# Kernel tuning notes

Hardware: AMD Instinct MI355X
Metric: run time of the kernel (lower is better)

## Reference

```python
import jax, jax.numpy as jnp
import numpy as np

B, DIM_IN, DIM_OUT, K, EMBED, N, S = 32, 32, 32, 2, 16, 2048, 12


def setup_inputs() -> dict:
    key = jax.random.key(0)
    ks = jax.random.split(key, 12)
    sc = 0.1
    return {
        "x": jax.random.normal(ks[0], (B, DIM_IN, N, S), dtype=jnp.float32),
        "node_embeddings": jax.random.normal(ks[1], (N, EMBED), dtype=jnp.float32),
        "node_embeddings2": jax.random.normal(ks[2], (N, EMBED), dtype=jnp.float32),
        "weights_pool": jax.random.normal(ks[3], (EMBED, K + 1, DIM_IN, DIM_OUT), dtype=jnp.float32) * sc,
        "weights_pool2": jax.random.normal(ks[4], (EMBED, K + 1, DIM_IN, DIM_OUT), dtype=jnp.float32) * sc,
        "bias_pool": jax.random.normal(ks[5], (EMBED, DIM_OUT), dtype=jnp.float32) * sc,
        "bias_pool2": jax.random.normal(ks[6], (EMBED, DIM_OUT), dtype=jnp.float32) * sc,
        "fc0_w": jax.random.normal(ks[7], (1, S), dtype=jnp.float32) * sc,
        "fc0_b": jnp.zeros((1,), dtype=jnp.float32),
        "fc1_w": jax.random.normal(ks[8], (EMBED, N), dtype=jnp.float32) * sc,
        "fc1_b": jnp.zeros((EMBED,), dtype=jnp.float32),
        "fc2_w": jax.random.normal(ks[9], (EMBED, DIM_IN), dtype=jnp.float32) * sc,
        "fc2_b": jnp.zeros((EMBED,), dtype=jnp.float32),
    }


def _mlp(x, fc0_w, fc0_b, fc1_w, fc1_b, fc2_w, fc2_b):
    # x: [B, i, n, s] -> use first batch element, as in the torch code
    h = x[0]                                        # [i, n, s]
    h = jnp.tanh((h @ fc0_w.T + fc0_b).squeeze(-1))  # [i, n]
    h = jnp.tanh(h @ fc1_w.T + fc1_b)                # [i, d]
    h = h.T                                          # [d, i]
    h = jnp.tanh(h @ fc2_w.T + fc2_b)                # [d, d]
    return h


def reference(x, node_embeddings, node_embeddings2, weights_pool, weights_pool2,
              bias_pool, bias_pool2, fc0_w, fc0_b, fc1_w, fc1_b, fc2_w, fc2_b):
    m = _mlp(x, fc0_w, fc0_b, fc1_w, fc1_b, fc2_w, fc2_b)          # [d, d]
    logits = jax.nn.relu((node_embeddings @ m) @ node_embeddings2.T)  # [n, n]
    support = jax.nn.softmax(logits, axis=1)                        # [n, n]

    # k-hop powers of the dynamic adjacency (k is a small static int)
    support_set = [jnp.eye(N, dtype=support.dtype)]
    for _ in range(K):
        support_set.append(support_set[-1] @ support)
    supports = jnp.stack(support_set, axis=0)                       # [K+1, n, n]

    # node-embedding-generated weights and bias
    weights = (jnp.einsum('nd,dkio->nkio', node_embeddings, weights_pool)
               + jnp.einsum('nd,dkio->nkio', node_embeddings2, weights_pool2))  # [n,K+1,i,o]
    bias = node_embeddings @ bias_pool + node_embeddings2 @ bias_pool2          # [n, o]

    x_g = jnp.einsum('knm,bims->bknis', supports, x)                # [b,K+1,n,i,s]
    x_gconv = jnp.einsum('bknis,nkio->bsno', x_g, weights) + bias   # [b,s,n,o]
    out = jnp.transpose(x_gconv, (0, 3, 2, 1))                      # [b,o,n,s]
    # dropout is identity in eval mode
    return out
```

## Files before the change

kernel.cpp:

```cpp
#include <hip/hip_runtime.h>


typedef float  f32x4  __attribute__((ext_vector_type(4)));
typedef __bf16 bf16x8 __attribute__((ext_vector_type(8)));
typedef unsigned short u16;

#define GLOAD16(gp, lp) __builtin_amdgcn_global_load_lds( \
    (const __attribute__((address_space(1))) void*)(gp),  \
    (__attribute__((address_space(3))) void*)(lp), 16, 0, 0)

__device__ __forceinline__ u16 f2bf(float f){
  union { float f; unsigned u; } v; v.f = f;
  unsigned u = v.u;
  u += 0x7fffu + ((u >> 16) & 1u);
  return (u16)(u >> 16);
}
__device__ __forceinline__ float bf2f(u16 h){
  union { unsigned u; float f; } v; v.u = ((unsigned)h) << 16;
  return v.f;
}
__device__ __forceinline__ float2 unp2(unsigned u){
  union { unsigned q; float f; } a, b;
  a.q = u << 16; b.q = u & 0xffff0000u;
  return make_float2(a.f, b.f);
}

__global__ void k_h1(const float* __restrict__ x, const float* __restrict__ fc0w,
                     const float* __restrict__ fc0b, float* __restrict__ h1){
  int g = blockIdx.x * 256 + threadIdx.x;
  const float* xp = x + (long)g * 12;
  float s = fc0b[0];
  #pragma unroll
  for (int j = 0; j < 12; j++) s += xp[j] * fc0w[j];
  h1[g] = tanhf(s);
}

__global__ __launch_bounds__(256) void k_h2a(const float* __restrict__ h1,
                                             const float* __restrict__ fc1w,
                                             float* __restrict__ h2raw){
  __shared__ float red[4];
  int id = blockIdx.x;
  int i = id >> 4, d = id & 15;
  int t = threadIdx.x;
  const float* hp = h1 + i * 2048;
  const float* wp = fc1w + d * 2048;
  float s = 0.f;
  for (int nn = t; nn < 2048; nn += 256) s += hp[nn] * wp[nn];
  for (int off = 32; off > 0; off >>= 1) s += __shfl_down(s, off, 64);
  if ((t & 63) == 0) red[t >> 6] = s;
  __syncthreads();
  if (t == 0) h2raw[id] = red[0] + red[1] + red[2] + red[3];
}

__global__ void k_h2b(const float* __restrict__ h2raw, const float* __restrict__ fc1b,
                      const float* __restrict__ fc2w, const float* __restrict__ fc2b,
                      float* __restrict__ mmat){
  __shared__ float h2[512];
  int t = threadIdx.x;
  {
    int d = t & 15;
    h2[t] = tanhf(h2raw[t] + fc1b[d]);
  }
  __syncthreads();
  if (t < 256){
    int dd = t >> 4, e = t & 15;
    float s2 = fc2b[e];
    #pragma unroll
    for (int ii = 0; ii < 32; ii++) s2 += h2[ii * 16 + dd] * fc2w[e * 32 + ii];
    mmat[dd * 16 + e] = tanhf(s2);
  }
}

__global__ __launch_bounds__(256) void k_support(const float* __restrict__ E1,
                                                 const float* __restrict__ E2,
                                                 const float* __restrict__ mmat,
                                                 u16* __restrict__ sup){
  __shared__ float ml[256];
  __shared__ float tv[16];
  __shared__ float red[8];
  int n = blockIdx.x, t = threadIdx.x;
  ml[t] = mmat[t];
  __syncthreads();
  if (t < 16){
    float s = 0.f;
    const float* er = E1 + n * 16;
    #pragma unroll
    for (int d = 0; d < 16; d++) s += er[d] * ml[d * 16 + t];
    tv[t] = s;
  }
  __syncthreads();
  float lmax = -1e30f;
  float lv[8];
  #pragma unroll
  for (int p = 0; p < 8; p++){
    int j = t + p * 256;
    const float* e2 = E2 + j * 16;
    float s = 0.f;
    #pragma unroll
    for (int d = 0; d < 16; d++) s += tv[d] * e2[d];
    s = fmaxf(s, 0.f);
    lv[p] = s;
    lmax = fmaxf(lmax, s);
  }
  for (int off = 32; off > 0; off >>= 1) lmax = fmaxf(lmax, __shfl_down(lmax, off, 64));
  if ((t & 63) == 0) red[t >> 6] = lmax;
  __syncthreads();
  if (t == 0) red[0] = fmaxf(fmaxf(red[0], red[1]), fmaxf(red[2], red[3]));
  __syncthreads();
  float mx = red[0];
  float lsum = 0.f;
  #pragma unroll
  for (int p = 0; p < 8; p++){ float e = __expf(lv[p] - mx); lv[p] = e; lsum += e; }
  for (int off = 32; off > 0; off >>= 1) lsum += __shfl_down(lsum, off, 64);
  if ((t & 63) == 0) red[4 + (t >> 6)] = lsum;
  __syncthreads();
  if (t == 0) red[4] = red[4] + red[5] + red[6] + red[7];
  __syncthreads();
  float inv = 1.f / red[4];
  #pragma unroll
  for (int p = 0; p < 8; p++) sup[(long)n * 2048 + t + p * 256] = f2bf(lv[p] * inv);
}

__global__ __launch_bounds__(256) void k_xbt2(const float* __restrict__ x,
                                              u16* __restrict__ Xb,
                                              u16* __restrict__ Xbt){
  __shared__ u16 tile[64][65];
  int cT = blockIdx.x * 64;
  int mT = blockIdx.y * 64;
  int t = threadIdx.x;
  int r = t >> 6, cc = t & 63;
  int cg = cT + cc;
  int bi = cg / 12, s = cg - bi * 12;
  long xoff = (long)bi * 24576 + s;
  #pragma unroll
  for (int p = 0; p < 16; p++){
    int rr = p * 4 + r;
    u16 v = f2bf(x[xoff + (long)(mT + rr) * 12]);
    tile[rr][cc] = v;
    Xb[(long)(mT + rr) * 12288 + cg] = v;
  }
  __syncthreads();
  #pragma unroll
  for (int p = 0; p < 16; p++){
    int rr = p * 4 + r;
    Xbt[(long)(cT + rr) * 2048 + mT + cc] = tile[cc][rr];
  }
}

__global__ __launch_bounds__(256) void k_wb2(const float* __restrict__ E1, const float* __restrict__ E2,
                                             const float* __restrict__ P1, const float* __restrict__ P2,
                                             const float* __restrict__ BP1, const float* __restrict__ BP2,
                                             float* __restrict__ W, float* __restrict__ biasN){
  int bid = blockIdx.x, t = threadIdx.x;
  if (bid < 6144){
    int nb = bid & 511, rb = bid >> 9;
    int n = nb * 4 + (t >> 6);
    int r4 = rb * 64 + (t & 63);
    const float* e1 = E1 + n * 16;
    const float* e2 = E2 + n * 16;
    f32x4 s = {0.f, 0.f, 0.f, 0.f};
    #pragma unroll
    for (int d = 0; d < 16; d++){
      f32x4 p1 = *(const f32x4*)(P1 + d * 3072 + r4 * 4);
      f32x4 p2 = *(const f32x4*)(P2 + d * 3072 + r4 * 4);
      s += p1 * e1[d] + p2 * e2[d];
    }
    *(f32x4*)(W + (long)n * 3072 + r4 * 4) = s;
  } else {
    int e = (bid - 6144) * 256 + t;
    int n = e >> 5, o = e & 31;
    const float* e1 = E1 + n * 16;
    const float* e2 = E2 + n * 16;
    float s = 0.f;
    #pragma unroll
    for (int d = 0; d < 16; d++) s += e1[d] * BP1[d * 32 + o] + e2[d] * BP2[d * 32 + o];
    biasN[e] = s;
  }
}

__global__ __launch_bounds__(512, 2) void k_gemm(const u16* __restrict__ A,
                                                 const u16* __restrict__ Bt,
                                                 u16* __restrict__ Cd,
                                                 u16* __restrict__ Ct,
                                                 int writeT){
  __shared__ u16 lds[65536];
  int tid  = threadIdx.x;
  int wave = tid >> 6, lane = tid & 63;
  int l15 = lane & 15, q = lane >> 4, l7 = l15 & 7;
  int wm = wave >> 2, wn = wave & 3;

  int lin  = blockIdx.y * 48 + blockIdx.x;
  int xcd  = lin & 7;
  int slot = lin >> 3;
  int yN   = slot / 6;
  int xN   = (slot - yN * 6) * 8 + xcd;
  long mBase = (long)yN * 256;
  long cBase = (long)xN * 256;

  f32x4 acc[8][4];
  #pragma unroll
  for (int t2 = 0; t2 < 8; t2++)
    #pragma unroll
    for (int u2 = 0; u2 < 4; u2++) acc[t2][u2] = (f32x4){0.f, 0.f, 0.f, 0.f};

  int Lrow = tid >> 3;
  int cel  = (tid & 7) ^ (Lrow & 7);
  const u16* gAp = A  + (mBase + Lrow) * 2048 + cel * 8;
  const u16* gBp = Bt + (cBase + Lrow) * 2048 + cel * 8;

#define GL_A(nx, ko, r) GLOAD16(gAp + (r) * (64 * 2048) + (ko), \
                                lds + (nx) + (r) * 4096 + wave * 512)
#define GL_B(nx, ko, r) GLOAD16(gBp + (r) * (64 * 2048) + (ko), \
                                lds + (nx) + 16384 + (r) * 4096 + wave * 512)

#define LDA(dst, mq) do { \
    _Pragma("unroll") \
    for (int t2 = 0; t2 < 4; t2++){ \
      int row = wm * 128 + ((mq) * 4 + t2) * 16 + l15; \
      _Pragma("unroll") \
      for (int kk = 0; kk < 2; kk++) \
        dst[t2][kk] = *(const bf16x8*)&lds[bA + row * 64 + (((kk << 2) | q) ^ l7) * 8]; \
    } } while(0)

#define LDB(nq) do { \
    _Pragma("unroll") \
    for (int u2 = 0; u2 < 2; u2++){ \
      int row = wn * 64 + ((nq) * 2 + u2) * 16 + l15; \
      _Pragma("unroll") \
      for (int kk = 0; kk < 2; kk++) \
        bb[u2][kk] = *(const bf16x8*)&lds[bB + row * 64 + (((kk << 2) | q) ^ l7) * 8]; \
    } } while(0)

#define MFMA_Q(AF, mq, nq) do { \
    __builtin_amdgcn_s_setprio(1); \
    _Pragma("unroll") \
    for (int t2 = 0; t2 < 4; t2++) \
      _Pragma("unroll") \
      for (int u2 = 0; u2 < 2; u2++) \
        _Pragma("unroll") \
        for (int kk = 0; kk < 2; kk++) \
          acc[(mq) * 4 + t2][(nq) * 2 + u2] = __builtin_amdgcn_mfma_f32_16x16x32_bf16( \
              AF[t2][kk], bb[u2][kk], acc[(mq) * 4 + t2][(nq) * 2 + u2], 0, 0, 0); \
    __builtin_amdgcn_s_setprio(0); \
  } while(0)

  GL_B(0, 0, 0); GL_B(0, 0, 1); GL_B(0, 0, 2); GL_B(0, 0, 3);
  GL_A(0, 0, 0); GL_A(0, 0, 2); GL_A(0, 0, 1); GL_A(0, 0, 3);

  for (int t = 0; t < 32; t++){
    const int bA = (t & 1) ? 32768 : 0;
    const int bB = bA + 16384;
    const int nx = (t & 1) ? 0 : 32768;
    const long ko = (long)(t + 1) * 64;
    bf16x8 aA[4][2], aB[4][2], bb[2][2];
    asm volatile("s_waitcnt vmcnt(0)" ::: "memory");
    __builtin_amdgcn_s_barrier();
    LDA(aA, 0);
    LDB(0);
    if (t < 31){ GL_B(nx, ko, 0); GL_B(nx, ko, 1); GL_B(nx, ko, 2); GL_B(nx, ko, 3); }
    __builtin_amdgcn_s_barrier();
    MFMA_Q(aA, 0, 0);
    __builtin_amdgcn_s_barrier();
    LDA(aB, 1);
    if (t < 31){ GL_A(nx, ko, 0); GL_A(nx, ko, 2); }
    __builtin_amdgcn_s_barrier();
    MFMA_Q(aB, 1, 0);
    __builtin_amdgcn_s_barrier();
    LDB(1);
    if (t < 31){ GL_A(nx, ko, 1); GL_A(nx, ko, 3); }
    __builtin_amdgcn_s_barrier();
    MFMA_Q(aB, 1, 1);
    __builtin_amdgcn_s_barrier();
    MFMA_Q(aA, 0, 1);
    __builtin_amdgcn_s_barrier();
  }
  asm volatile("s_waitcnt vmcnt(0)" ::: "memory");
  __syncthreads();

  #pragma unroll
  for (int t2 = 0; t2 < 8; t2++){
    int m0 = wm * 128 + t2 * 16 + q * 4;
    #pragma unroll
    for (int u2 = 0; u2 < 4; u2++){
      int c = wn * 64 + u2 * 16 + l15;
      ushort4 v = make_ushort4(f2bf(acc[t2][u2][0]), f2bf(acc[t2][u2][1]),
                               f2bf(acc[t2][u2][2]), f2bf(acc[t2][u2][3]));
      int sw = ((m0 >> 3) ^ (c & 7) ^ ((c >> 3) & 7));
      *(ushort4*)&lds[c * 256 + (sw << 3) + (m0 & 7)] = v;
    }
  }
  __syncthreads();
  int rr = tid >> 5;
  int ch = tid & 31;
  if (writeT){
    #pragma unroll
    for (int p = 0; p < 16; p++){
      int r = p * 16 + rr;
      uint4 v = *(const uint4*)&lds[r * 256 + ((ch ^ (r & 7) ^ ((r >> 3) & 7)) << 3)];
      *(uint4*)&Ct[(cBase + r) * 2048 + mBase + ch * 8] = v;
    }
  }
  #pragma unroll
  for (int p = 0; p < 16; p++){
    int m = p * 16 + rr;
    int msw = (m >> 3), ml = m & 7;
    unsigned w[4];
    #pragma unroll
    for (int jj = 0; jj < 4; jj++){
      int c0 = ch * 8 + jj * 2, c1 = c0 + 1;
      unsigned lo = lds[c0 * 256 + (((msw ^ (c0 & 7) ^ (ch & 7)) << 3)) + ml];
      unsigned hi = lds[c1 * 256 + (((msw ^ (c1 & 7) ^ (ch & 7)) << 3)) + ml];
      w[jj] = lo | (hi << 16);
    }
    uint4 v = make_uint4(w[0], w[1], w[2], w[3]);
    *(uint4*)&Cd[(mBase + m) * 12288 + cBase + ch * 8] = v;
  }
#undef GL_A
#undef GL_B
#undef LDA
#undef LDB
#undef MFMA_Q
}

__global__ __launch_bounds__(256, 4) void k_final(const u16* __restrict__ G0,
                                                  const u16* __restrict__ G1,
                                                  const u16* __restrict__ G2,
                                                  const float* __restrict__ W,
                                                  const float* __restrict__ biasN,
                                                  float* __restrict__ out){
  __shared__ __align__(16) u16 gs[32 * 400];
  __shared__ __align__(16) float ws4[1024];
  __shared__ float bbuf[32];
  int bid = blockIdx.x;
  int n = (bid & 7) * 256 + (bid >> 3);
  int t = threadIdx.x;
  int b = t >> 3, oc = t & 7;
  f32x4 acc[4][3];
  #pragma unroll
  for (int jo = 0; jo < 4; jo++)
    #pragma unroll
    for (int v = 0; v < 3; v++) acc[jo][v] = (f32x4){0.f, 0.f, 0.f, 0.f};

  const u16* srcs[3] = {G0, G1, G2};
  for (int k = 0; k < 3; k++){
    __syncthreads();
    const uint4* src = (const uint4*)(srcs[k] + (long)n * 12288);
    #pragma unroll
    for (int p = 0; p < 6; p++){
      int c = t + p * 256;
      int br = c / 48, wi = c - br * 48;
      *(uint4*)&gs[br * 400 + wi * 8] = src[c];
    }
    const float4* wsrc = (const float4*)(W + (long)n * 3072 + k * 1024);
    *(float4*)&ws4[t * 4] = wsrc[t];
    if (k == 0 && t < 8) *(float4*)&bbuf[t * 4] = ((const float4*)(biasN + (long)n * 32))[t];
    __syncthreads();

    const u16* gp = gs + b * 400;
    #pragma unroll 4
    for (int ii = 0; ii < 16; ii++){
      uint4 A  = *(const uint4*)&gp[ii * 24];
      uint4 Bc = *(const uint4*)&gp[ii * 24 + 8];
      uint4 Cc = *(const uint4*)&gp[ii * 24 + 16];
      float2 p0 = unp2(A.x),  p1 = unp2(A.y),  p2 = unp2(A.z),  p3 = unp2(A.w);
      float2 p4 = unp2(Bc.x), p5 = unp2(Bc.y), p6 = unp2(Bc.z), p7 = unp2(Bc.w);
      float2 p8 = unp2(Cc.x), p9 = unp2(Cc.y), pa = unp2(Cc.z), pb = unp2(Cc.w);
      f32x4 G0v0 = (f32x4){p0.x, p0.y, p1.x, p1.y};
      f32x4 G0v1 = (f32x4){p2.x, p2.y, p3.x, p3.y};
      f32x4 G0v2 = (f32x4){p4.x, p4.y, p5.x, p5.y};
      f32x4 G1v0 = (f32x4){p6.x, p6.y, p7.x, p7.y};
      f32x4 G1v1 = (f32x4){p8.x, p8.y, p9.x, p9.y};
      f32x4 G1v2 = (f32x4){pa.x, pa.y, pb.x, pb.y};
      #pragma unroll
      for (int jo = 0; jo < 4; jo++){
        float w0 = ws4[(ii * 2)     * 32 + oc + jo * 8];
        float w1 = ws4[(ii * 2 + 1) * 32 + oc + jo * 8];
        acc[jo][0] += G0v0 * w0;
        acc[jo][1] += G0v1 * w0;
        acc[jo][2] += G0v2 * w0;
        acc[jo][0] += G1v0 * w1;
        acc[jo][1] += G1v1 * w1;
        acc[jo][2] += G1v2 * w1;
      }
    }
  }
  #pragma unroll
  for (int jo = 0; jo < 4; jo++){
    int o = oc + jo * 8;
    float bv = bbuf[o];
    f32x4 bs = {bv, bv, bv, bv};
    long base = ((long)(b * 32 + o) * 2048 + n) * 12;
    *(f32x4*)(out + base)     = acc[jo][0] + bs;
    *(f32x4*)(out + base + 4) = acc[jo][1] + bs;
    *(f32x4*)(out + base + 8) = acc[jo][2] + bs;
  }
}

extern "C" void kernel_launch(void* const* d_in, const int* in_sizes, int n_in,
                              void* d_out, int out_size, void* d_ws, size_t ws_size,
                              hipStream_t stream){
  const float* x    = (const float*)d_in[0];
  const float* E1   = (const float*)d_in[1];
  const float* E2   = (const float*)d_in[2];
  const float* P1   = (const float*)d_in[3];
  const float* P2   = (const float*)d_in[4];
  const float* BP1  = (const float*)d_in[5];
  const float* BP2  = (const float*)d_in[6];
  const float* fc0w = (const float*)d_in[7];
  const float* fc0b = (const float*)d_in[8];
  const float* fc1w = (const float*)d_in[9];
  const float* fc1b = (const float*)d_in[10];
  const float* fc2w = (const float*)d_in[11];
  const float* fc2b = (const float*)d_in[12];
  float* out = (float*)d_out;

  char* ws = (char*)d_ws;
  size_t off = 0;
  auto carve = [&](size_t bytes) -> char* {
    char* p = ws + off;
    off += (bytes + 255) & ~(size_t)255;
    return p;
  };
  float* h1            = (float*)carve((size_t)65536 * 4);
  float* h2raw         = (float*)carve((size_t)512 * 4);
  float* mmat          = (float*)carve((size_t)256 * 4);
  u16* sup             = (u16*)carve((size_t)2048 * 2048 * 2);
  u16* Xbt             = (u16*)carve((size_t)12288 * 2048 * 2);
  u16* Xb              = (u16*)carve((size_t)2048 * 12288 * 2);
  u16* G1t             = (u16*)carve((size_t)12288 * 2048 * 2);
  u16* G1              = (u16*)carve((size_t)2048 * 12288 * 2);
  float* W             = (float*)carve((size_t)2048 * 3072 * 4);
  float* biasN         = (float*)carve((size_t)2048 * 32 * 4);
  u16* G2              = Xbt;
  (void)ws_size; (void)in_sizes; (void)n_in; (void)out_size;

  k_h1     <<<256, 256, 0, stream>>>(x, fc0w, fc0b, h1);
  k_h2a    <<<512, 256, 0, stream>>>(h1, fc1w, h2raw);
  k_h2b    <<<1, 512, 0, stream>>>(h2raw, fc1b, fc2w, fc2b, mmat);
  k_support<<<2048, 256, 0, stream>>>(E1, E2, mmat, sup);
  k_xbt2   <<<dim3(192, 32), 256, 0, stream>>>(x, Xb, Xbt);
  k_wb2    <<<6400, 256, 0, stream>>>(E1, E2, P1, P2, BP1, BP2, W, biasN);
  k_gemm   <<<dim3(48, 8), 512, 0, stream>>>(sup, Xbt, G1, G1t, 1);
  k_gemm   <<<dim3(48, 8), 512, 0, stream>>>(sup, G1t, G2, G1t, 0);
  k_final  <<<2048, 256, 0, stream>>>(Xb, G1, G2, W, biasN, out);
}
```

Measured before the change: 615.8 us.

## Enlarge GEMM tile to 256x384 for a single-wave grid with finer load waits

The bf16 support GEMM tile grows from 256x256 to 256x384, so each launch uses 256 blocks instead of 384. On a 256-CU part this removes the 1.5-wave tail, and each loaded A tile is reused over more columns. The main loop now uses partial vmcnt waits so the second-half A rows can still be arriving while the first half is consumed. The epilogue writes output in two 192-column halves to fit the LDS staging buffer. In exchange, LDS use rises to 160 KB, which allows only one block per CU. Register pressure also grows with 192 accumulator VGPRs, and the last iteration issues redundant wrapped loads.

```diff
diff --git a/kernel.cpp b/kernel.cpp
--- a/kernel.cpp
+++ b/kernel.cpp
@@ -183,25 +183,25 @@
                                                  u16* __restrict__ Cd,
                                                  u16* __restrict__ Ct,
                                                  int writeT){
-  __shared__ u16 lds[65536];
+  __shared__ u16 lds[81920];
   int tid  = threadIdx.x;
   int wave = tid >> 6, lane = tid & 63;
   int l15 = lane & 15, q = lane >> 4, l7 = l15 & 7;
   int wm = wave >> 2, wn = wave & 3;
 
-  int lin  = blockIdx.y * 48 + blockIdx.x;
+  int lin  = blockIdx.y * 32 + blockIdx.x;
   int xcd  = lin & 7;
   int slot = lin >> 3;
-  int yN   = slot / 6;
-  int xN   = (slot - yN * 6) * 8 + xcd;
+  int yN   = slot >> 2;
+  int xN   = (slot & 3) * 8 + xcd;
   long mBase = (long)yN * 256;
-  long cBase = (long)xN * 256;
-
-  f32x4 acc[8][4];
+  long cBase = (long)xN * 384;
+
+  f32x4 acc[8][6];
   #pragma unroll
   for (int t2 = 0; t2 < 8; t2++)
     #pragma unroll
-    for (int u2 = 0; u2 < 4; u2++) acc[t2][u2] = (f32x4){0.f, 0.f, 0.f, 0.f};
+    for (int u2 = 0; u2 < 6; u2++) acc[t2][u2] = (f32x4){0.f, 0.f, 0.f, 0.f};
 
   int Lrow = tid >> 3;
   int cel  = (tid & 7) ^ (Lrow & 7);
@@ -222,16 +222,16 @@
         dst[t2][kk] = *(const bf16x8*)&lds[bA + row * 64 + (((kk << 2) | q) ^ l7) * 8]; \
     } } while(0)
 
-#define LDB(nq) do { \
+#define LDB(dst, nq2) do { \
     _Pragma("unroll") \
     for (int u2 = 0; u2 < 2; u2++){ \
-      int row = wn * 64 + ((nq) * 2 + u2) * 16 + l15; \
+      int row = wn * 96 + ((nq2) * 2 + u2) * 16 + l15; \
       _Pragma("unroll") \
       for (int kk = 0; kk < 2; kk++) \
-        bb[u2][kk] = *(const bf16x8*)&lds[bB + row * 64 + (((kk << 2) | q) ^ l7) * 8]; \
+        dst[u2][kk] = *(const bf16x8*)&lds[bB + row * 64 + (((kk << 2) | q) ^ l7) * 8]; \
     } } while(0)
 
-#define MFMA_Q(AF, mq, nq) do { \
+#define MFMA_Q(AF, mq, BB, nb) do { \
     __builtin_amdgcn_s_setprio(1); \
     _Pragma("unroll") \
     for (int t2 = 0; t2 < 4; t2++) \
@@ -239,81 +239,100 @@
       for (int u2 = 0; u2 < 2; u2++) \
         _Pragma("unroll") \
         for (int kk = 0; kk < 2; kk++) \
-          acc[(mq) * 4 + t2][(nq) * 2 + u2] = __builtin_amdgcn_mfma_f32_16x16x32_bf16( \
-              AF[t2][kk], bb[u2][kk], acc[(mq) * 4 + t2][(nq) * 2 + u2], 0, 0, 0); \
+          acc[(mq) * 4 + t2][(nb) + u2] = __builtin_amdgcn_mfma_f32_16x16x32_bf16( \
+              AF[t2][kk], BB[u2][kk], acc[(mq) * 4 + t2][(nb) + u2], 0, 0, 0); \
     __builtin_amdgcn_s_setprio(0); \
   } while(0)
 
-  GL_B(0, 0, 0); GL_B(0, 0, 1); GL_B(0, 0, 2); GL_B(0, 0, 3);
+  GL_B(0, 0, 0); GL_B(0, 0, 1); GL_B(0, 0, 2);
+  GL_B(0, 0, 3); GL_B(0, 0, 4); GL_B(0, 0, 5);
   GL_A(0, 0, 0); GL_A(0, 0, 2); GL_A(0, 0, 1); GL_A(0, 0, 3);
 
   for (int t = 0; t < 32; t++){
-    const int bA = (t & 1) ? 32768 : 0;
+    const int bA = (t & 1) ? 40960 : 0;
     const int bB = bA + 16384;
-    const int nx = (t & 1) ? 0 : 32768;
-    const long ko = (long)(t + 1) * 64;
-    bf16x8 aA[4][2], aB[4][2], bb[2][2];
-    asm volatile("s_waitcnt vmcnt(0)" ::: "memory");
-    __builtin_amdgcn_s_barrier();
-    LDA(aA, 0);
-    LDB(0);
-    if (t < 31){ GL_B(nx, ko, 0); GL_B(nx, ko, 1); GL_B(nx, ko, 2); GL_B(nx, ko, 3); }
-    __builtin_amdgcn_s_barrier();
-    MFMA_Q(aA, 0, 0);
-    __builtin_amdgcn_s_barrier();
-    LDA(aB, 1);
-    if (t < 31){ GL_A(nx, ko, 0); GL_A(nx, ko, 2); }
-    __builtin_amdgcn_s_barrier();
-    MFMA_Q(aB, 1, 0);
-    __builtin_amdgcn_s_barrier();
-    LDB(1);
-    if (t < 31){ GL_A(nx, ko, 1); GL_A(nx, ko, 3); }
-    __builtin_amdgcn_s_barrier();
-    MFMA_Q(aB, 1, 1);
-    __builtin_amdgcn_s_barrier();
-    MFMA_Q(aA, 0, 1);
-    __builtin_amdgcn_s_barrier();
+    const int nx = (t & 1) ? 0 : 40960;
+    const long ko = (long)((t + 1) & 31) * 64;
+    bf16x8 aA0[4][2], aA1[4][2], bb0[2][2], bb1[2][2], bb2[2][2];
+    asm volatile("s_waitcnt vmcnt(2)" ::: "memory");
+    __builtin_amdgcn_s_barrier();
+    LDA(aA0, 0);
+    LDB(bb0, 0);
+    GL_B(nx, ko, 0); GL_B(nx, ko, 1);
+    __builtin_amdgcn_s_barrier();
+    MFMA_Q(aA0, 0, bb0, 0);
+    __builtin_amdgcn_s_barrier();
+    LDB(bb1, 1);
+    GL_B(nx, ko, 2); GL_B(nx, ko, 3);
+    __builtin_amdgcn_s_barrier();
+    MFMA_Q(aA0, 0, bb1, 2);
+    __builtin_amdgcn_s_barrier();
+    LDB(bb2, 2);
+    GL_B(nx, ko, 4); GL_B(nx, ko, 5);
+    __builtin_amdgcn_s_barrier();
+    MFMA_Q(aA0, 0, bb2, 4);
+    asm volatile("s_waitcnt vmcnt(6)" ::: "memory");
+    __builtin_amdgcn_s_barrier();
+    LDA(aA1, 1);
+    GL_A(nx, ko, 0); GL_A(nx, ko, 2);
+    __builtin_amdgcn_s_barrier();
+    MFMA_Q(aA1, 1, bb2, 4);
+    __builtin_amdgcn_s_barrier();
+    GL_A(nx, ko, 1); GL_A(nx, ko, 3);
+    __builtin_amdgcn_s_barrier();
+    MFMA_Q(aA1, 1, bb1, 2);
+    __builtin_amdgcn_s_barrier();
+    MFMA_Q(aA1, 1, bb0, 0);
   }
   asm volatile("s_waitcnt vmcnt(0)" ::: "memory");
-  __syncthreads();
-
-  #pragma unroll
-  for (int t2 = 0; t2 < 8; t2++){
-    int m0 = wm * 128 + t2 * 16 + q * 4;
-    #pragma unroll
-    for (int u2 = 0; u2 < 4; u2++){
-      int c = wn * 64 + u2 * 16 + l15;
-      ushort4 v = make_ushort4(f2bf(acc[t2][u2][0]), f2bf(acc[t2][u2][1]),
-                               f2bf(acc[t2][u2][2]), f2bf(acc[t2][u2][3]));
-      int sw = ((m0 >> 3) ^ (c & 7) ^ ((c >> 3) & 7));
-      *(ushort4*)&lds[c * 256 + (sw << 3) + (m0 & 7)] = v;
-    }
-  }
-  __syncthreads();
-  int rr = tid >> 5;
-  int ch = tid & 31;
-  if (writeT){
-    #pragma unroll
-    for (int p = 0; p < 16; p++){
-      int r = p * 16 + rr;
-      uint4 v = *(const uint4*)&lds[r * 256 + ((ch ^ (r & 7) ^ ((r >> 3) & 7)) << 3)];
-      *(uint4*)&Ct[(cBase + r) * 2048 + mBase + ch * 8] = v;
-    }
-  }
-  #pragma unroll
-  for (int p = 0; p < 16; p++){
-    int m = p * 16 + rr;
-    int msw = (m >> 3), ml = m & 7;
-    unsigned w[4];
-    #pragma unroll
-    for (int jj = 0; jj < 4; jj++){
-      int c0 = ch * 8 + jj * 2, c1 = c0 + 1;
-      unsigned lo = lds[c0 * 256 + (((msw ^ (c0 & 7) ^ (ch & 7)) << 3)) + ml];
-      unsigned hi = lds[c1 * 256 + (((msw ^ (c1 & 7) ^ (ch & 7)) << 3)) + ml];
-      w[jj] = lo | (hi << 16);
-    }
-    uint4 v = make_uint4(w[0], w[1], w[2], w[3]);
-    *(uint4*)&Cd[(mBase + m) * 12288 + cBase + ch * 8] = v;
+  __builtin_amdgcn_sched_barrier(0);
+  __syncthreads();
+
+  for (int hc = 0; hc < 2; hc++){
+    if (hc) __syncthreads();
+    if ((wn >> 1) == hc){
+      int wnl = wn & 1;
+      #pragma unroll
+      for (int t2 = 0; t2 < 8; t2++){
+        int m0 = wm * 128 + t2 * 16 + q * 4;
+        #pragma unroll
+        for (int u2 = 0; u2 < 6; u2++){
+          int lc = wnl * 96 + u2 * 16 + l15;
+          ushort4 v = make_ushort4(f2bf(acc[t2][u2][0]), f2bf(acc[t2][u2][1]),
+                                   f2bf(acc[t2][u2][2]), f2bf(acc[t2][u2][3]));
+          int sw = ((m0 >> 3) ^ (lc & 7) ^ ((lc >> 3) & 7));
+          *(ushort4*)&lds[lc * 256 + (sw << 3) + (m0 & 7)] = v;
+        }
+      }
+    }
+    __syncthreads();
+    int rr = tid >> 5;
+    int ch = tid & 31;
+    if (writeT){
+      #pragma unroll
+      for (int p = 0; p < 12; p++){
+        int r = p * 16 + rr;
+        uint4 v = *(const uint4*)&lds[r * 256 + ((ch ^ (r & 7) ^ ((r >> 3) & 7)) << 3)];
+        *(uint4*)&Ct[(cBase + hc * 192 + r) * 2048 + mBase + ch * 8] = v;
+      }
+    }
+    if (ch < 24){
+      #pragma unroll
+      for (int p = 0; p < 16; p++){
+        int m = p * 16 + rr;
+        int msw = (m >> 3), ml = m & 7;
+        unsigned w[4];
+        #pragma unroll
+        for (int jj = 0; jj < 4; jj++){
+          int c0 = ch * 8 + jj * 2, c1 = c0 + 1;
+          unsigned lo = lds[c0 * 256 + (((msw ^ (c0 & 7) ^ (ch & 7)) << 3)) + ml];
+          unsigned hi = lds[c1 * 256 + (((msw ^ (c1 & 7) ^ (ch & 7)) << 3)) + ml];
+          w[jj] = lo | (hi << 16);
+        }
+        uint4 v = make_uint4(w[0], w[1], w[2], w[3]);
+        *(uint4*)&Cd[(mBase + m) * 12288 + cBase + hc * 192 + ch * 8] = v;
+      }
+    }
   }
 #undef GL_A
 #undef GL_B
@@ -440,7 +459,7 @@
   k_support<<<2048, 256, 0, stream>>>(E1, E2, mmat, sup);
   k_xbt2   <<<dim3(192, 32), 256, 0, stream>>>(x, Xb, Xbt);
   k_wb2    <<<6400, 256, 0, stream>>>(E1, E2, P1, P2, BP1, BP2, W, biasN);
-  k_gemm   <<<dim3(48, 8), 512, 0, stream>>>(sup, Xbt, G1, G1t, 1);
-  k_gemm   <<<dim3(48, 8), 512, 0, stream>>>(sup, G1t, G2, G1t, 0);
+  k_gemm   <<<dim3(32, 8), 512, 0, stream>>>(sup, Xbt, G1, G1t, 1);
+  k_gemm   <<<dim3(32, 8), 512, 0, stream>>>(sup, G1t, G2, G1t, 0);
   k_final  <<<2048, 256, 0, stream>>>(Xb, G1, G2, W, biasN, out);
 }
```

After: 1.068 ms. +73.4%, slower.
